# Kernel tuning notes

Hardware: AMD Instinct MI355X
Metric: run time of the kernel (lower is better)

Reference implementation:

```python
import jax, jax.numpy as jnp
import numpy as np

EMBED = 1024
HEADS = 16
HEAD_DIM = EMBED // HEADS


def setup_inputs() -> dict:
    key = jax.random.key(0)
    k1, k2, k3, k4, k5 = jax.random.split(key, 5)
    B, S = 4, 2048
    scale = 1.0 / np.sqrt(EMBED)
    return {
        "query_features": jax.random.normal(k1, (B, S, EMBED), dtype=jnp.float32),
        "W_qkv": jax.random.normal(k2, (EMBED, 3 * EMBED), dtype=jnp.float32) * scale,
        "b_qkv": jnp.zeros((3 * EMBED,), dtype=jnp.float32),
        "W_out": jax.random.normal(k3, (EMBED, EMBED), dtype=jnp.float32) * scale,
        "b_out": jnp.zeros((EMBED,), dtype=jnp.float32),
    }


def reference(query_features, W_qkv, b_qkv, W_out, b_out):
    B, S, E = query_features.shape
    qkv = jnp.einsum("bse,ef->bsf", query_features, W_qkv) + b_qkv  # [B,S,3E]
    q, k, v = jnp.split(qkv, 3, axis=-1)
    # split heads: [B,H,S,D]
    def heads(x):
        return x.reshape(B, S, HEADS, HEAD_DIM).transpose(0, 2, 1, 3)
    q, k, v = heads(q), heads(k), heads(v)
    scale = 1.0 / np.sqrt(HEAD_DIM)
    scores = jnp.einsum("bhqd,bhkd->bhqk", q, k) * scale
    attn = jax.nn.softmax(scores, axis=-1)
    out = jnp.einsum("bhqk,bhkd->bhqd", attn, v)  # [B,H,S,D]
    out = out.transpose(0, 2, 1, 3).reshape(B, S, E)
    return jnp.einsum("bse,ef->bsf", out, W_out) + b_out
```

## Files before the change

kernel.cpp:

```cpp
#include <hip/hip_runtime.h>
#include <hip/hip_bf16.h>
#include <stdint.h>
#include <stddef.h>

using short8  = __attribute__((ext_vector_type(8))) short;
using short4v = __attribute__((ext_vector_type(4))) short;
using int4v   = __attribute__((ext_vector_type(4))) int;
using f32x4   = __attribute__((ext_vector_type(4))) float;
typedef __hip_bfloat16 bf16_t;

__device__ __forceinline__ void glds16(const void* g, const void* l) {
  __builtin_amdgcn_global_load_lds(
      (const __attribute__((address_space(1))) void*)g,
      (__attribute__((address_space(3))) void*)l, 16, 0, 0);
}
__device__ __forceinline__ short bfbits(float x) {
  bf16_t h = __float2bfloat16(x);
  return __builtin_bit_cast(short, h);
}
__device__ __forceinline__ int pk2(float lo, float hi) {
  return __builtin_amdgcn_perm(__builtin_bit_cast(unsigned, hi),
                               __builtin_bit_cast(unsigned, lo), 0x07060302u);
}

__global__ void dtype_probe(const unsigned short* __restrict__ w, int* flag) {
  __shared__ int sbad;
  const int tid = threadIdx.x;
  if (tid == 0) sbad = 0;
  __syncthreads();
  int bad = 0;
  for (int i = tid; i < 4096; i += 256) {
    float f = __uint_as_float((unsigned)w[i] << 16);
    if (!(fabsf(f) <= 1e10f)) bad = 1;
  }
  if (bad) sbad = 1;
  __syncthreads();
  if (tid == 0) *flag = sbad;
}

__global__ __launch_bounds__(256)
void transpose_both(const void* __restrict__ Wqkv, bf16_t* __restrict__ WqkvT,
                    const void* __restrict__ Wout, bf16_t* __restrict__ WoutT,
                    const int* __restrict__ flag) {
  __shared__ float tile[32][33];
  const int tx = threadIdx.x, ty = threadIdx.y;
  int bx = blockIdx.x;
  const void* Wv;
  bf16_t* Wt;
  int C;
  if (bx < 96) {
    Wv = Wqkv; Wt = WqkvT; C = 3072;
  } else {
    bx -= 96; Wv = Wout; Wt = WoutT; C = 1024;
  }
  const int n0 = bx * 32, k0 = blockIdx.y * 32;
  const int isf = *flag;
#pragma unroll
  for (int j = 0; j < 4; ++j) {
    const int k = k0 + ty + j * 8;
    tile[ty + j * 8][tx] =
        isf ? ((const float*)Wv)[(size_t)k * C + n0 + tx]
            : __bfloat162float(((const bf16_t*)Wv)[(size_t)k * C + n0 + tx]);
  }
  __syncthreads();
#pragma unroll
  for (int j = 0; j < 4; ++j) {
    const int n = n0 + ty + j * 8;
    Wt[(size_t)n * 1024 + k0 + tx] = __float2bfloat16(tile[tx][ty + j * 8]);
  }
}

__global__ __launch_bounds__(256)
void convert_x(const void* __restrict__ Xv, bf16_t* __restrict__ Xb, int total,
               const int* __restrict__ flag) {
  const int i = (blockIdx.x * 256 + threadIdx.x) * 4;
  if (i >= total) return;
  if (*flag) {
    const float4 v = *(const float4*)((const float*)Xv + i);
    Xb[i + 0] = __float2bfloat16(v.x);
    Xb[i + 1] = __float2bfloat16(v.y);
    Xb[i + 2] = __float2bfloat16(v.z);
    Xb[i + 3] = __float2bfloat16(v.w);
  } else {
    *(uint2*)(Xb + i) = *(const uint2*)((const bf16_t*)Xv + i);
  }
}

template <int MODE>
__global__ __launch_bounds__(512, 2)
void gemm_k(const bf16_t* __restrict__ A, const bf16_t* __restrict__ Bt,
            const void* __restrict__ biasv, void* __restrict__ Cv,
            bf16_t* __restrict__ Qo, bf16_t* __restrict__ Ko,
            bf16_t* __restrict__ Vo, int M, int N, int K,
            const int* __restrict__ flag) {
  constexpr float CSC = 0.18033688011112042f;
  __shared__ __align__(16) bf16_t lds[8 * 8192];

  const int isf32 = *flag;
  const int tid  = threadIdx.x;
  const int w    = tid >> 6;
  const int lane = tid & 63;
  const int lrow = lane & 15;
  const int quad = lane >> 4;
  const int wr   = w >> 2;
  const int wc   = w & 3;
  const int m0 = blockIdx.x * 256;
  const int n0 = blockIdx.y * 256;
  const int fk  = lrow & 7;
  const int sl0 = ((0 + quad) ^ fk) << 4;
  const int sl1 = ((4 + quad) ^ fk) << 4;
  const int NT = K >> 6;

  f32x4 acc[8][4];
#pragma unroll
  for (int i = 0; i < 8; ++i)
#pragma unroll
    for (int j = 0; j < 4; ++j)
#pragma unroll
      for (int r = 0; r < 4; ++r) acc[i][j][r] = 0.f;

  auto stage = [&](int n) {
    if (n >= 4 * NT) return;
    const int slot = n & 7;
    const int part = n & 3;
    const int kt   = (n >> 2) << 6;
    const bf16_t* src = (part < 2) ? A : Bt;
    const int rb = ((part < 2) ? m0 : n0) + ((part & 1) << 7);
#pragma unroll
    for (int i = 0; i < 2; ++i) {
      const int cbase = i * 512 + w * 64;
      const int c = cbase + lane;
      const int row = c >> 3, ch = c & 7;
      glds16(src + (size_t)(rb + row) * K + kt + ((ch ^ (row & 7)) << 3),
             (const char*)lds + slot * 16384 + cbase * 16);
    }
  };

  const char* ldsc = (const char*)lds;
  const int aoff = (wr << 14) + (lrow << 7);
  const int boff = ((2 + (wc >> 1)) << 14) + ((((wc & 1) << 6) + lrow) << 7);

#pragma unroll
  for (int n = 0; n < 5; ++n) stage(n);
  asm volatile("s_waitcnt vmcnt(2)" ::: "memory");
  __builtin_amdgcn_s_barrier();

  for (int t = 0; t < NT; ++t) {
    const int qb = (t & 1) << 16;

    short8 al[4], b0[4];
#pragma unroll
    for (int mi = 0; mi < 4; ++mi)
      al[mi] = *(const short8*)(ldsc + qb + aoff + mi * 2048 + sl0);
#pragma unroll
    for (int ni = 0; ni < 4; ++ni)
      b0[ni] = *(const short8*)(ldsc + qb + boff + ni * 2048 + sl0);
    stage(4 * t + 5);
    __builtin_amdgcn_s_barrier();
    __builtin_amdgcn_s_setprio(1);
#pragma unroll
    for (int mi = 0; mi < 4; ++mi)
#pragma unroll
      for (int ni = 0; ni < 4; ++ni)
        acc[mi][ni] = __builtin_amdgcn_mfma_f32_16x16x32_bf16(
            al[mi], b0[ni], acc[mi][ni], 0, 0, 0);
    __builtin_amdgcn_s_setprio(0);
    __builtin_amdgcn_s_barrier();

    short8 ah[4], b1[4];
#pragma unroll
    for (int mi = 0; mi < 4; ++mi)
      ah[mi] = *(const short8*)(ldsc + qb + aoff + (mi + 4) * 2048 + sl0);
#pragma unroll
    for (int ni = 0; ni < 4; ++ni)
      b1[ni] = *(const short8*)(ldsc + qb + boff + ni * 2048 + sl1);
    stage(4 * t + 6);
    __builtin_amdgcn_s_barrier();
    __builtin_amdgcn_s_setprio(1);
#pragma unroll
    for (int mi = 0; mi < 4; ++mi)
#pragma unroll
      for (int ni = 0; ni < 4; ++ni)
        acc[mi + 4][ni] = __builtin_amdgcn_mfma_f32_16x16x32_bf16(
            ah[mi], b0[ni], acc[mi + 4][ni], 0, 0, 0);
    __builtin_amdgcn_s_setprio(0);
    __builtin_amdgcn_s_barrier();

    short8 al1[4], ah1[4];
#pragma unroll
    for (int mi = 0; mi < 4; ++mi)
      al1[mi] = *(const short8*)(ldsc + qb + aoff + mi * 2048 + sl1);
#pragma unroll
    for (int mi = 0; mi < 4; ++mi)
      ah1[mi] = *(const short8*)(ldsc + qb + aoff + (mi + 4) * 2048 + sl1);
    stage(4 * t + 7);
    __builtin_amdgcn_s_barrier();
    __builtin_amdgcn_s_setprio(1);
#pragma unroll
    for (int mi = 0; mi < 4; ++mi)
#pragma unroll
      for (int ni = 0; ni < 4; ++ni)
        acc[mi][ni] = __builtin_amdgcn_mfma_f32_16x16x32_bf16(
            al1[mi], b1[ni], acc[mi][ni], 0, 0, 0);
    __builtin_amdgcn_s_setprio(0);
    asm volatile("s_waitcnt lgkmcnt(0)" ::: "memory");
    __builtin_amdgcn_s_barrier();

    stage(4 * t + 8);
    asm volatile("s_waitcnt vmcnt(2)" ::: "memory");
    __builtin_amdgcn_s_barrier();
    __builtin_amdgcn_s_setprio(1);
#pragma unroll
    for (int mi = 0; mi < 4; ++mi)
#pragma unroll
      for (int ni = 0; ni < 4; ++ni)
        acc[mi + 4][ni] = __builtin_amdgcn_mfma_f32_16x16x32_bf16(
            ah1[mi], b1[ni], acc[mi + 4][ni], 0, 0, 0);
    __builtin_amdgcn_s_setprio(0);
    __builtin_amdgcn_s_barrier();
  }

  if (MODE == 1) {
    const int sec = n0 >> 10;
    const int b = m0 >> 11;
    const int s0 = (m0 & 2047) + wr * 128 + quad * 4;
#pragma unroll
    for (int mi = 0; mi < 8; ++mi) {
      const int s = s0 + mi * 16;
#pragma unroll
      for (int ni = 0; ni < 4; ++ni) {
        const int col = n0 + wc * 64 + ni * 16 + lrow;
        const float bv = isf32 ? ((const float*)biasv)[col]
                               : __bfloat162float(((const bf16_t*)biasv)[col]);
        const int h = (col >> 6) & 15, d = col & 63;
        if (sec == 2) {
          short4v hv4;
#pragma unroll
          for (int r = 0; r < 4; ++r) hv4[r] = bfbits(acc[mi][ni][r] + bv);
          *(short4v*)(Vo + ((((size_t)b * 16 + h) * 64) + d) * 2048 + s) = hv4;
        } else if (sec == 0) {
          bf16_t* dst = Qo + ((((size_t)b * 16 + h) * 2048) + s) * 64 + d;
#pragma unroll
          for (int r = 0; r < 4; ++r)
            dst[(size_t)r * 64] = __float2bfloat16((acc[mi][ni][r] + bv) * CSC);
        } else {
          bf16_t* dst = Ko + ((((size_t)b * 16 + h) * 2048) + s) * 64 + d;
#pragma unroll
          for (int r = 0; r < 4; ++r)
            dst[(size_t)r * 64] = __float2bfloat16(acc[mi][ni][r] + bv);
        }
      }
    }
  } else {
#pragma unroll
    for (int mi = 0; mi < 8; ++mi) {
#pragma unroll
      for (int ni = 0; ni < 4; ++ni) {
        const int col = n0 + wc * 64 + ni * 16 + lrow;
        const float bv = isf32 ? ((const float*)biasv)[col]
                               : __bfloat162float(((const bf16_t*)biasv)[col]);
#pragma unroll
        for (int r = 0; r < 4; ++r) {
          const int row = m0 + wr * 128 + mi * 16 + quad * 4 + r;
          const float val = acc[mi][ni][r] + bv;
          if (isf32)
            ((float*)Cv)[(size_t)row * N + col] = val;
          else
            ((bf16_t*)Cv)[(size_t)row * N + col] = __float2bfloat16(val);
        }
      }
    }
  }
}

__global__ __launch_bounds__(256, 3)
void attn_fwd(const bf16_t* __restrict__ Q, const bf16_t* __restrict__ K,
              const bf16_t* __restrict__ Vt, bf16_t* __restrict__ AO) {
  __shared__ __align__(16) bf16_t lK[2][64 * 64];
  __shared__ __align__(16) bf16_t lV[2][64 * 64];

  const int tid  = threadIdx.x;
  const int w    = tid >> 6;
  const int lane = tid & 63;
  const int lrow = lane & 15;
  const int quad = lane >> 4;
  const int id = blockIdx.x;
  const int bh = (id & 7) * 8 + (id >> 7);
  const int q0 = ((id >> 3) & 15) * 128;

  const bf16_t* Qb = Q + (size_t)bh * 2048 * 64;
  const bf16_t* Kb = K + (size_t)bh * 2048 * 64;
  const bf16_t* Vb = Vt + (size_t)bh * 64 * 2048;

  const int rbase = (lrow >> 2) * 8 + (lrow & 3);
  const int fkl   = 2 * (lrow >> 2) + (lrow & 1);

  short8 aq[2][2];
#pragma unroll
  for (int qt = 0; qt < 2; ++qt)
#pragma unroll
    for (int ks = 0; ks < 2; ++ks)
      aq[qt][ks] = *(const short8*)(Qb +
          (size_t)(q0 + w * 32 + qt * 16 + lrow) * 64 + ks * 32 + quad * 8);

  short8 ones;
#pragma unroll
  for (int j = 0; j < 8; ++j) ones[j] = (short)0x3F80;

  f32x4 ot[4][2];
  f32x4 lsacc[2];
#pragma unroll
  for (int dt = 0; dt < 4; ++dt)
    for (int qt = 0; qt < 2; ++qt)
      for (int r = 0; r < 4; ++r) ot[dt][qt][r] = 0.f;
  for (int qt = 0; qt < 2; ++qt)
    for (int r = 0; r < 4; ++r) lsacc[qt][r] = 0.f;

  auto stage = [&](int buf, int kt) {
#pragma unroll
    for (int i = 0; i < 2; ++i) {
      const int cbase = i * 256 + w * 64;
      const int c = cbase + lane;
      const int row = c >> 3, ch = c & 7;
      const int fk = 2 * ((row >> 3) & 3) + (row & 1);
      glds16(Kb + (size_t)(kt + row) * 64 + (ch ^ fk) * 8,
             (const char*)lK[buf] + cbase * 16);
      glds16(Vb + (size_t)row * 2048 + kt + (ch ^ (row & 7)) * 8,
             (const char*)lV[buf] + cbase * 16);
    }
  };

  auto compute = [&](const bf16_t* lKb, const bf16_t* lVb) {
    f32x4 sc[2][2][2];
#pragma unroll
    for (int g = 0; g < 2; ++g)
      for (int T = 0; T < 2; ++T)
        for (int qt = 0; qt < 2; ++qt)
          for (int r = 0; r < 4; ++r) sc[g][T][qt][r] = 0.f;
#pragma unroll
    for (int ks = 0; ks < 2; ++ks) {
      short8 ak[2][2];
#pragma unroll
      for (int g = 0; g < 2; ++g)
#pragma unroll
        for (int T = 0; T < 2; ++T) {
          const int row = g * 32 + T * 4 + rbase;
          const int slot = (ks * 4 + quad) ^ fkl;
          ak[g][T] =
              *(const short8*)((const char*)lKb + row * 128 + slot * 16);
        }
#pragma unroll
      for (int g = 0; g < 2; ++g)
#pragma unroll
        for (int T = 0; T < 2; ++T)
#pragma unroll
          for (int qt = 0; qt < 2; ++qt)
            sc[g][T][qt] = __builtin_amdgcn_mfma_f32_16x16x32_bf16(
                ak[g][T], aq[qt][ks], sc[g][T][qt], 0, 0, 0);
    }
#pragma unroll
    for (int g = 0; g < 2; ++g) {
      short8 pb[2];
#pragma unroll
      for (int qt = 0; qt < 2; ++qt) {
        float p[8];
#pragma unroll
        for (int T = 0; T < 2; ++T)
#pragma unroll
          for (int r = 0; r < 4; ++r)
            p[T * 4 + r] = __builtin_amdgcn_exp2f(sc[g][T][qt][r]);
        int4v pi = {pk2(p[0], p[1]), pk2(p[2], p[3]), pk2(p[4], p[5]),
                    pk2(p[6], p[7])};
        pb[qt] = __builtin_bit_cast(short8, pi);
        lsacc[qt] = __builtin_amdgcn_mfma_f32_16x16x32_bf16(ones, pb[qt],
                                                            lsacc[qt], 0, 0, 0);
      }
#pragma unroll
      for (int dt = 0; dt < 4; ++dt) {
        const int row = dt * 16 + lrow;
        const int slot = (g * 4 + quad) ^ (row & 7);
        const short8 vf =
            *(const short8*)((const char*)lVb + row * 128 + slot * 16);
#pragma unroll
        for (int qt = 0; qt < 2; ++qt)
          ot[dt][qt] = __builtin_amdgcn_mfma_f32_16x16x32_bf16(
              vf, pb[qt], ot[dt][qt], 0, 0, 0);
      }
    }
  };

  stage(0, 0);
  __syncthreads();

  for (int kt = 0; kt < 2048; kt += 128) {
    if (kt + 64 < 2048) stage(1, kt + 64);
    compute(lK[0], lV[0]);
    __syncthreads();
    if (kt + 128 < 2048) stage(0, kt + 128);
    compute(lK[1], lV[1]);
    __syncthreads();
  }

  const int b = bh >> 4, h = bh & 15;
#pragma unroll
  for (int qt = 0; qt < 2; ++qt) {
    const float inv = 1.f / lsacc[qt][0];
    const int srow = q0 + w * 32 + qt * 16 + lrow;
#pragma unroll
    for (int dt = 0; dt < 4; ++dt) {
      uint2 pack;
      short* ps = (short*)&pack;
#pragma unroll
      for (int r = 0; r < 4; ++r) ps[r] = bfbits(ot[dt][qt][r] * inv);
      *(uint2*)(AO + ((size_t)b * 2048 + srow) * 1024 + h * 64 + dt * 16 +
                quad * 4) = pack;
    }
  }
}

extern "C" void kernel_launch(void* const* d_in, const int* in_sizes, int n_in,
                              void* d_out, int out_size, void* d_ws,
                              size_t ws_size, hipStream_t stream) {
  const void* X    = d_in[0];
  const void* Wqkv = d_in[1];
  const void* bqkv = d_in[2];
  const void* Wout = d_in[3];
  const void* bout = d_in[4];

  char* ws = (char*)d_ws;
  bf16_t* WqkvT = (bf16_t*)(ws);
  bf16_t* WoutT = (bf16_t*)(ws + 6291456);
  bf16_t* Qw    = (bf16_t*)(ws + 8388608);
  bf16_t* Kw    = (bf16_t*)(ws + 25165824);
  bf16_t* Vw    = (bf16_t*)(ws + 41943040);
  bf16_t* AOw   = (bf16_t*)(ws + 58720256);
  bf16_t* Xbf   = AOw;
  int*    flag  = (int*)(ws + 75497472);

  dtype_probe<<<1, 256, 0, stream>>>((const unsigned short*)Wqkv, flag);
  transpose_both<<<dim3(128, 32), dim3(32, 8), 0, stream>>>(Wqkv, WqkvT, Wout,
                                                            WoutT, flag);
  convert_x<<<8192, 256, 0, stream>>>(X, Xbf, 8388608, flag);

  gemm_k<1><<<dim3(32, 12), 512, 0, stream>>>(Xbf, WqkvT, bqkv, nullptr, Qw,
                                              Kw, Vw, 8192, 3072, 1024, flag);
  attn_fwd<<<1024, 256, 0, stream>>>(Qw, Kw, Vw, AOw);
  gemm_k<0><<<dim3(32, 4), 512, 0, stream>>>(AOw, WoutT, bout, d_out, nullptr,
                                             nullptr, nullptr, 8192, 1024, 1024,
                                             flag);
}
```

Measured before the change: 285.3 us.

## Fuse preprocessing kernels, simplify GEMM to 128x128 tiles, widen attention query tile

The dtype probe, weight transpose and input conversion are merged into one preprocess launch, with every block re-running the probe itself. The heavily pipelined 256x256 GEMM with an 8-slot prefetch ring is replaced by a simple single-buffered 128x128 tile loop using 256 threads. Each attention block now covers 256 query rows with 4 query tiles per wave, which raises K/V reuse and register pressure (occupancy hint lowered from 3 to 2). The simpler GEMM loses load/compute overlap, while the fused preprocess removes two launches.

```diff
diff --git a/kernel.cpp b/kernel.cpp
--- a/kernel.cpp
+++ b/kernel.cpp
@@ -23,78 +23,81 @@
                                __builtin_bit_cast(unsigned, lo), 0x07060302u);
 }
 
-__global__ void dtype_probe(const unsigned short* __restrict__ w, int* flag) {
+__global__ __launch_bounds__(256)
+void preprocess(const void* __restrict__ Wqkv, bf16_t* __restrict__ WqkvT,
+                const void* __restrict__ Wout, bf16_t* __restrict__ WoutT,
+                const void* __restrict__ Xv, bf16_t* __restrict__ Xb,
+                int* __restrict__ flag) {
   __shared__ int sbad;
+  __shared__ float tile[32][33];
   const int tid = threadIdx.x;
+  const int bid = blockIdx.x;
   if (tid == 0) sbad = 0;
   __syncthreads();
-  int bad = 0;
-  for (int i = tid; i < 4096; i += 256) {
-    float f = __uint_as_float((unsigned)w[i] << 16);
-    if (!(fabsf(f) <= 1e10f)) bad = 1;
-  }
-  if (bad) sbad = 1;
+  {
+    int bad = 0;
+    const unsigned short* wp = (const unsigned short*)Wqkv;
+#pragma unroll
+    for (int j = 0; j < 4; ++j) {
+      float f = __uint_as_float((unsigned)wp[tid + j * 256] << 16);
+      if (!(fabsf(f) <= 1e10f)) bad = 1;
+    }
+    if (bad) sbad = 1;
+  }
   __syncthreads();
-  if (tid == 0) *flag = sbad;
-}
-
+  const int isf = sbad;
+  if (bid == 0 && tid == 0) *flag = isf;
+
+  if (bid < 4096) {
+    int bx = bid & 127;
+    const int by = bid >> 7;
+    const int tx = tid & 31, ty = tid >> 5;
+    const void* Wv;
+    bf16_t* Wt;
+    int C;
+    if (bx < 96) {
+      Wv = Wqkv; Wt = WqkvT; C = 3072;
+    } else {
+      bx -= 96; Wv = Wout; Wt = WoutT; C = 1024;
+    }
+    const int n0 = bx * 32, k0 = by * 32;
+#pragma unroll
+    for (int j = 0; j < 4; ++j) {
+      const int k = k0 + ty + j * 8;
+      tile[ty + j * 8][tx] =
+          isf ? ((const float*)Wv)[(size_t)k * C + n0 + tx]
+              : __bfloat162float(((const bf16_t*)Wv)[(size_t)k * C + n0 + tx]);
+    }
+    __syncthreads();
+#pragma unroll
+    for (int j = 0; j < 4; ++j) {
+      const int n = n0 + ty + j * 8;
+      Wt[(size_t)n * 1024 + k0 + tx] = __float2bfloat16(tile[tx][ty + j * 8]);
+    }
+  } else {
+    const int i = ((bid - 4096) * 256 + tid) * 4;
+    if (isf) {
+      const float4 v = *(const float4*)((const float*)Xv + i);
+      Xb[i + 0] = __float2bfloat16(v.x);
+      Xb[i + 1] = __float2bfloat16(v.y);
+      Xb[i + 2] = __float2bfloat16(v.z);
+      Xb[i + 3] = __float2bfloat16(v.w);
+    } else {
+      *(uint2*)(Xb + i) = *(const uint2*)((const bf16_t*)Xv + i);
+    }
+  }
+}
+
+template <int MODE>
 __global__ __launch_bounds__(256)
-void transpose_both(const void* __restrict__ Wqkv, bf16_t* __restrict__ WqkvT,
-                    const void* __restrict__ Wout, bf16_t* __restrict__ WoutT,
-                    const int* __restrict__ flag) {
-  __shared__ float tile[32][33];
-  const int tx = threadIdx.x, ty = threadIdx.y;
-  int bx = blockIdx.x;
-  const void* Wv;
-  bf16_t* Wt;
-  int C;
-  if (bx < 96) {
-    Wv = Wqkv; Wt = WqkvT; C = 3072;
-  } else {
-    bx -= 96; Wv = Wout; Wt = WoutT; C = 1024;
-  }
-  const int n0 = bx * 32, k0 = blockIdx.y * 32;
-  const int isf = *flag;
-#pragma unroll
-  for (int j = 0; j < 4; ++j) {
-    const int k = k0 + ty + j * 8;
-    tile[ty + j * 8][tx] =
-        isf ? ((const float*)Wv)[(size_t)k * C + n0 + tx]
-            : __bfloat162float(((const bf16_t*)Wv)[(size_t)k * C + n0 + tx]);
-  }
-  __syncthreads();
-#pragma unroll
-  for (int j = 0; j < 4; ++j) {
-    const int n = n0 + ty + j * 8;
-    Wt[(size_t)n * 1024 + k0 + tx] = __float2bfloat16(tile[tx][ty + j * 8]);
-  }
-}
-
-__global__ __launch_bounds__(256)
-void convert_x(const void* __restrict__ Xv, bf16_t* __restrict__ Xb, int total,
-               const int* __restrict__ flag) {
-  const int i = (blockIdx.x * 256 + threadIdx.x) * 4;
-  if (i >= total) return;
-  if (*flag) {
-    const float4 v = *(const float4*)((const float*)Xv + i);
-    Xb[i + 0] = __float2bfloat16(v.x);
-    Xb[i + 1] = __float2bfloat16(v.y);
-    Xb[i + 2] = __float2bfloat16(v.z);
-    Xb[i + 3] = __float2bfloat16(v.w);
-  } else {
-    *(uint2*)(Xb + i) = *(const uint2*)((const bf16_t*)Xv + i);
-  }
-}
-
-template <int MODE>
-__global__ __launch_bounds__(512, 2)
 void gemm_k(const bf16_t* __restrict__ A, const bf16_t* __restrict__ Bt,
             const void* __restrict__ biasv, void* __restrict__ Cv,
             bf16_t* __restrict__ Qo, bf16_t* __restrict__ Ko,
             bf16_t* __restrict__ Vo, int M, int N, int K,
             const int* __restrict__ flag) {
   constexpr float CSC = 0.18033688011112042f;
-  __shared__ __align__(16) bf16_t lds[8 * 8192];
+  __shared__ __align__(16) bf16_t lA[128 * 64];
+  __shared__ __align__(16) bf16_t lB[128 * 64];
 
   const int isf32 = *flag;
   const int tid  = threadIdx.x;
@@ -102,137 +105,67 @@
   const int lane = tid & 63;
   const int lrow = lane & 15;
   const int quad = lane >> 4;
-  const int wr   = w >> 2;
-  const int wc   = w & 3;
-  const int m0 = blockIdx.x * 256;
-  const int n0 = blockIdx.y * 256;
-  const int fk  = lrow & 7;
-  const int sl0 = ((0 + quad) ^ fk) << 4;
-  const int sl1 = ((4 + quad) ^ fk) << 4;
-  const int NT = K >> 6;
-
-  f32x4 acc[8][4];
-#pragma unroll
-  for (int i = 0; i < 8; ++i)
-#pragma unroll
+  const int m0 = blockIdx.x * 128;
+  const int n0 = blockIdx.y * 128;
+  const int wm = (w >> 1) * 64;
+  const int wn = (w & 1) * 64;
+
+  f32x4 acc[4][4];
+  for (int i = 0; i < 4; ++i)
     for (int j = 0; j < 4; ++j)
-#pragma unroll
       for (int r = 0; r < 4; ++r) acc[i][j][r] = 0.f;
 
-  auto stage = [&](int n) {
-    if (n >= 4 * NT) return;
-    const int slot = n & 7;
-    const int part = n & 3;
-    const int kt   = (n >> 2) << 6;
-    const bf16_t* src = (part < 2) ? A : Bt;
-    const int rb = ((part < 2) ? m0 : n0) + ((part & 1) << 7);
-#pragma unroll
-    for (int i = 0; i < 2; ++i) {
-      const int cbase = i * 512 + w * 64;
+  for (int kt = 0; kt < K; kt += 64) {
+#pragma unroll
+    for (int i = 0; i < 4; ++i) {
+      const int cbase = i * 256 + w * 64;
       const int c = cbase + lane;
-      const int row = c >> 3, ch = c & 7;
-      glds16(src + (size_t)(rb + row) * K + kt + ((ch ^ (row & 7)) << 3),
-             (const char*)lds + slot * 16384 + cbase * 16);
-    }
-  };
-
-  const char* ldsc = (const char*)lds;
-  const int aoff = (wr << 14) + (lrow << 7);
-  const int boff = ((2 + (wc >> 1)) << 14) + ((((wc & 1) << 6) + lrow) << 7);
-
-#pragma unroll
-  for (int n = 0; n < 5; ++n) stage(n);
-  asm volatile("s_waitcnt vmcnt(2)" ::: "memory");
-  __builtin_amdgcn_s_barrier();
-
-  for (int t = 0; t < NT; ++t) {
-    const int qb = (t & 1) << 16;
-
-    short8 al[4], b0[4];
-#pragma unroll
-    for (int mi = 0; mi < 4; ++mi)
-      al[mi] = *(const short8*)(ldsc + qb + aoff + mi * 2048 + sl0);
-#pragma unroll
-    for (int ni = 0; ni < 4; ++ni)
-      b0[ni] = *(const short8*)(ldsc + qb + boff + ni * 2048 + sl0);
-    stage(4 * t + 5);
-    __builtin_amdgcn_s_barrier();
-    __builtin_amdgcn_s_setprio(1);
-#pragma unroll
-    for (int mi = 0; mi < 4; ++mi)
-#pragma unroll
-      for (int ni = 0; ni < 4; ++ni)
-        acc[mi][ni] = __builtin_amdgcn_mfma_f32_16x16x32_bf16(
-            al[mi], b0[ni], acc[mi][ni], 0, 0, 0);
-    __builtin_amdgcn_s_setprio(0);
-    __builtin_amdgcn_s_barrier();
-
-    short8 ah[4], b1[4];
-#pragma unroll
-    for (int mi = 0; mi < 4; ++mi)
-      ah[mi] = *(const short8*)(ldsc + qb + aoff + (mi + 4) * 2048 + sl0);
-#pragma unroll
-    for (int ni = 0; ni < 4; ++ni)
-      b1[ni] = *(const short8*)(ldsc + qb + boff + ni * 2048 + sl1);
-    stage(4 * t + 6);
-    __builtin_amdgcn_s_barrier();
-    __builtin_amdgcn_s_setprio(1);
-#pragma unroll
-    for (int mi = 0; mi < 4; ++mi)
-#pragma unroll
-      for (int ni = 0; ni < 4; ++ni)
-        acc[mi + 4][ni] = __builtin_amdgcn_mfma_f32_16x16x32_bf16(
-            ah[mi], b0[ni], acc[mi + 4][ni], 0, 0, 0);
-    __builtin_amdgcn_s_setprio(0);
-    __builtin_amdgcn_s_barrier();
-
-    short8 al1[4], ah1[4];
-#pragma unroll
-    for (int mi = 0; mi < 4; ++mi)
-      al1[mi] = *(const short8*)(ldsc + qb + aoff + mi * 2048 + sl1);
-#pragma unroll
-    for (int mi = 0; mi < 4; ++mi)
-      ah1[mi] = *(const short8*)(ldsc + qb + aoff + (mi + 4) * 2048 + sl1);
-    stage(4 * t + 7);
-    __builtin_amdgcn_s_barrier();
-    __builtin_amdgcn_s_setprio(1);
-#pragma unroll
-    for (int mi = 0; mi < 4; ++mi)
-#pragma unroll
-      for (int ni = 0; ni < 4; ++ni)
-        acc[mi][ni] = __builtin_amdgcn_mfma_f32_16x16x32_bf16(
-            al1[mi], b1[ni], acc[mi][ni], 0, 0, 0);
-    __builtin_amdgcn_s_setprio(0);
-    asm volatile("s_waitcnt lgkmcnt(0)" ::: "memory");
-    __builtin_amdgcn_s_barrier();
-
-    stage(4 * t + 8);
-    asm volatile("s_waitcnt vmcnt(2)" ::: "memory");
-    __builtin_amdgcn_s_barrier();
-    __builtin_amdgcn_s_setprio(1);
-#pragma unroll
-    for (int mi = 0; mi < 4; ++mi)
-#pragma unroll
-      for (int ni = 0; ni < 4; ++ni)
-        acc[mi + 4][ni] = __builtin_amdgcn_mfma_f32_16x16x32_bf16(
-            ah1[mi], b1[ni], acc[mi + 4][ni], 0, 0, 0);
-    __builtin_amdgcn_s_setprio(0);
-    __builtin_amdgcn_s_barrier();
+      const int row = c >> 3;
+      const int q = (c & 7) ^ (row & 7);
+      glds16(A + (size_t)(m0 + row) * K + kt + q * 8,
+             (const char*)lA + cbase * 16);
+      glds16(Bt + (size_t)(n0 + row) * K + kt + q * 8,
+             (const char*)lB + cbase * 16);
+    }
+    __syncthreads();
+#pragma unroll
+    for (int ks = 0; ks < 2; ++ks) {
+      short8 af[4], bfr[4];
+#pragma unroll
+      for (int mi = 0; mi < 4; ++mi) {
+        const int row = wm + mi * 16 + lrow;
+        const int slot = (ks * 4 + quad) ^ (row & 7);
+        af[mi] = *(const short8*)((const char*)lA + row * 128 + slot * 16);
+      }
+#pragma unroll
+      for (int ni = 0; ni < 4; ++ni) {
+        const int row = wn + ni * 16 + lrow;
+        const int slot = (ks * 4 + quad) ^ (row & 7);
+        bfr[ni] = *(const short8*)((const char*)lB + row * 128 + slot * 16);
+      }
+#pragma unroll
+      for (int mi = 0; mi < 4; ++mi)
+#pragma unroll
+        for (int ni = 0; ni < 4; ++ni)
+          acc[mi][ni] = __builtin_amdgcn_mfma_f32_16x16x32_bf16(
+              af[mi], bfr[ni], acc[mi][ni], 0, 0, 0);
+    }
+    __syncthreads();
   }
 
   if (MODE == 1) {
     const int sec = n0 >> 10;
     const int b = m0 >> 11;
-    const int s0 = (m0 & 2047) + wr * 128 + quad * 4;
-#pragma unroll
-    for (int mi = 0; mi < 8; ++mi) {
-      const int s = s0 + mi * 16;
+    const int s0 = (m0 & 2047) + wm + quad * 4;
+#pragma unroll
+    for (int mi = 0; mi < 4; ++mi) {
 #pragma unroll
       for (int ni = 0; ni < 4; ++ni) {
-        const int col = n0 + wc * 64 + ni * 16 + lrow;
+        const int col = n0 + wn + ni * 16 + lrow;
         const float bv = isf32 ? ((const float*)biasv)[col]
                                : __bfloat162float(((const bf16_t*)biasv)[col]);
         const int h = (col >> 6) & 15, d = col & 63;
+        const int s = s0 + mi * 16;
         if (sec == 2) {
           short4v hv4;
 #pragma unroll
@@ -253,15 +186,15 @@
     }
   } else {
 #pragma unroll
-    for (int mi = 0; mi < 8; ++mi) {
+    for (int mi = 0; mi < 4; ++mi) {
 #pragma unroll
       for (int ni = 0; ni < 4; ++ni) {
-        const int col = n0 + wc * 64 + ni * 16 + lrow;
+        const int col = n0 + wn + ni * 16 + lrow;
         const float bv = isf32 ? ((const float*)biasv)[col]
                                : __bfloat162float(((const bf16_t*)biasv)[col]);
 #pragma unroll
         for (int r = 0; r < 4; ++r) {
-          const int row = m0 + wr * 128 + mi * 16 + quad * 4 + r;
+          const int row = m0 + wm + mi * 16 + quad * 4 + r;
           const float val = acc[mi][ni][r] + bv;
           if (isf32)
             ((float*)Cv)[(size_t)row * N + col] = val;
@@ -273,7 +206,7 @@
   }
 }
 
-__global__ __launch_bounds__(256, 3)
+__global__ __launch_bounds__(256, 2)
 void attn_fwd(const bf16_t* __restrict__ Q, const bf16_t* __restrict__ K,
               const bf16_t* __restrict__ Vt, bf16_t* __restrict__ AO) {
   __shared__ __align__(16) bf16_t lK[2][64 * 64];
@@ -285,8 +218,9 @@
   const int lrow = lane & 15;
   const int quad = lane >> 4;
   const int id = blockIdx.x;
-  const int bh = (id & 7) * 8 + (id >> 7);
-  const int q0 = ((id >> 3) & 15) * 128;
+  const int swz = (id & 7) * 64 + (id >> 3);
+  const int bh  = swz >> 3;
+  const int q0  = (swz & 7) * 256;
 
   const bf16_t* Qb = Q + (size_t)bh * 2048 * 64;
   const bf16_t* Kb = K + (size_t)bh * 2048 * 64;
@@ -295,25 +229,29 @@
   const int rbase = (lrow >> 2) * 8 + (lrow & 3);
   const int fkl   = 2 * (lrow >> 2) + (lrow & 1);
 
-  short8 aq[2][2];
-#pragma unroll
-  for (int qt = 0; qt < 2; ++qt)
+  short8 aq[4][2];
+#pragma unroll
+  for (int qt = 0; qt < 4; ++qt)
 #pragma unroll
     for (int ks = 0; ks < 2; ++ks)
       aq[qt][ks] = *(const short8*)(Qb +
-          (size_t)(q0 + w * 32 + qt * 16 + lrow) * 64 + ks * 32 + quad * 8);
+          (size_t)(q0 + w * 64 + qt * 16 + lrow) * 64 + ks * 32 + quad * 8);
 
   short8 ones;
 #pragma unroll
   for (int j = 0; j < 8; ++j) ones[j] = (short)0x3F80;
 
-  f32x4 ot[4][2];
-  f32x4 lsacc[2];
+  f32x4 ot[4][4];
+  f32x4 lsacc[4];
 #pragma unroll
   for (int dt = 0; dt < 4; ++dt)
-    for (int qt = 0; qt < 2; ++qt)
+#pragma unroll
+    for (int qt = 0; qt < 4; ++qt)
+#pragma unroll
       for (int r = 0; r < 4; ++r) ot[dt][qt][r] = 0.f;
-  for (int qt = 0; qt < 2; ++qt)
+#pragma unroll
+  for (int qt = 0; qt < 4; ++qt)
+#pragma unroll
     for (int r = 0; r < 4; ++r) lsacc[qt][r] = 0.f;
 
   auto stage = [&](int buf, int kt) {
@@ -331,44 +269,40 @@
   };
 
   auto compute = [&](const bf16_t* lKb, const bf16_t* lVb) {
-    f32x4 sc[2][2][2];
-#pragma unroll
-    for (int g = 0; g < 2; ++g)
+#pragma unroll
+    for (int g = 0; g < 2; ++g) {
+      f32x4 sc[2][4];
+#pragma unroll
       for (int T = 0; T < 2; ++T)
-        for (int qt = 0; qt < 2; ++qt)
-          for (int r = 0; r < 4; ++r) sc[g][T][qt][r] = 0.f;
-#pragma unroll
-    for (int ks = 0; ks < 2; ++ks) {
-      short8 ak[2][2];
-#pragma unroll
-      for (int g = 0; g < 2; ++g)
+#pragma unroll
+        for (int qt = 0; qt < 4; ++qt)
+#pragma unroll
+          for (int r = 0; r < 4; ++r) sc[T][qt][r] = 0.f;
+#pragma unroll
+      for (int ks = 0; ks < 2; ++ks) {
+        short8 ak[2];
 #pragma unroll
         for (int T = 0; T < 2; ++T) {
           const int row = g * 32 + T * 4 + rbase;
           const int slot = (ks * 4 + quad) ^ fkl;
-          ak[g][T] =
-              *(const short8*)((const char*)lKb + row * 128 + slot * 16);
+          ak[T] = *(const short8*)((const char*)lKb + row * 128 + slot * 16);
         }
 #pragma unroll
-      for (int g = 0; g < 2; ++g)
-#pragma unroll
         for (int T = 0; T < 2; ++T)
 #pragma unroll
-          for (int qt = 0; qt < 2; ++qt)
-            sc[g][T][qt] = __builtin_amdgcn_mfma_f32_16x16x32_bf16(
-                ak[g][T], aq[qt][ks], sc[g][T][qt], 0, 0, 0);
-    }
-#pragma unroll
-    for (int g = 0; g < 2; ++g) {
-      short8 pb[2];
-#pragma unroll
-      for (int qt = 0; qt < 2; ++qt) {
+          for (int qt = 0; qt < 4; ++qt)
+            sc[T][qt] = __builtin_amdgcn_mfma_f32_16x16x32_bf16(
+                ak[T], aq[qt][ks], sc[T][qt], 0, 0, 0);
+      }
+      short8 pb[4];
+#pragma unroll
+      for (int qt = 0; qt < 4; ++qt) {
         float p[8];
 #pragma unroll
         for (int T = 0; T < 2; ++T)
 #pragma unroll
           for (int r = 0; r < 4; ++r)
-            p[T * 4 + r] = __builtin_amdgcn_exp2f(sc[g][T][qt][r]);
+            p[T * 4 + r] = __builtin_amdgcn_exp2f(sc[T][qt][r]);
         int4v pi = {pk2(p[0], p[1]), pk2(p[2], p[3]), pk2(p[4], p[5]),
                     pk2(p[6], p[7])};
         pb[qt] = __builtin_bit_cast(short8, pi);
@@ -382,7 +316,7 @@
         const short8 vf =
             *(const short8*)((const char*)lVb + row * 128 + slot * 16);
 #pragma unroll
-        for (int qt = 0; qt < 2; ++qt)
+        for (int qt = 0; qt < 4; ++qt)
           ot[dt][qt] = __builtin_amdgcn_mfma_f32_16x16x32_bf16(
               vf, pb[qt], ot[dt][qt], 0, 0, 0);
       }
@@ -403,9 +337,9 @@
 
   const int b = bh >> 4, h = bh & 15;
 #pragma unroll
-  for (int qt = 0; qt < 2; ++qt) {
+  for (int qt = 0; qt < 4; ++qt) {
     const float inv = 1.f / lsacc[qt][0];
-    const int srow = q0 + w * 32 + qt * 16 + lrow;
+    const int srow = q0 + w * 64 + qt * 16 + lrow;
 #pragma unroll
     for (int dt = 0; dt < 4; ++dt) {
       uint2 pack;
@@ -437,15 +371,12 @@
   bf16_t* Xbf   = AOw;
   int*    flag  = (int*)(ws + 75497472);
 
-  dtype_probe<<<1, 256, 0, stream>>>((const unsigned short*)Wqkv, flag);
-  transpose_both<<<dim3(128, 32), dim3(32, 8), 0, stream>>>(Wqkv, WqkvT, Wout,
-                                                            WoutT, flag);
-  convert_x<<<8192, 256, 0, stream>>>(X, Xbf, 8388608, flag);
-
-  gemm_k<1><<<dim3(32, 12), 512, 0, stream>>>(Xbf, WqkvT, bqkv, nullptr, Qw,
+  preprocess<<<12288, 256, 0, stream>>>(Wqkv, WqkvT, Wout, WoutT, X, Xbf, flag);
+
+  gemm_k<1><<<dim3(64, 24), 256, 0, stream>>>(Xbf, WqkvT, bqkv, nullptr, Qw,
                                               Kw, Vw, 8192, 3072, 1024, flag);
-  attn_fwd<<<1024, 256, 0, stream>>>(Qw, Kw, Vw, AOw);
-  gemm_k<0><<<dim3(32, 4), 512, 0, stream>>>(AOw, WoutT, bout, d_out, nullptr,
+  attn_fwd<<<512, 256, 0, stream>>>(Qw, Kw, Vw, AOw);
+  gemm_k<0><<<dim3(64, 8), 256, 0, stream>>>(AOw, WoutT, bout, d_out, nullptr,
                                              nullptr, nullptr, 8192, 1024, 1024,
                                              flag);
 }
```

Result: faster. 255.9 us (-10.3%).
